# Performance work log

Hardware: AMD Instinct MI355X
Metric: run time of the kernel (lower is better)

The kernel has to match this reference:

```python
import jax, jax.numpy as jnp
import numpy as np

N_NODES = 100000
N_EDGES = 600000
VOCAB = 5000
NUM_GRAPHS = 2000
NUM_CLASSES = 10


def setup_inputs() -> dict:
    key = jax.random.key(0)
    ks = jax.random.split(key, 12)
    x = jax.random.randint(ks[0], (N_NODES,), 0, VOCAB, dtype=jnp.int32)
    edge_index = jax.random.randint(ks[1], (2, N_EDGES), 0, N_NODES, dtype=jnp.int32)
    batch = jnp.sort(jax.random.randint(ks[2], (N_NODES,), 0, NUM_GRAPHS, dtype=jnp.int32))
    emb = jax.random.normal(ks[3], (VOCAB, 64), dtype=jnp.float32) * 0.1
    W1 = jax.random.normal(ks[4], (64, 128), dtype=jnp.float32) * (1.0 / np.sqrt(64))
    b1 = jnp.zeros((128,), dtype=jnp.float32)
    W2 = jax.random.normal(ks[5], (128, 128), dtype=jnp.float32) * (1.0 / np.sqrt(128))
    b2 = jnp.zeros((128,), dtype=jnp.float32)
    Wlin = jax.random.normal(ks[6], (128, NUM_CLASSES), dtype=jnp.float32) * (1.0 / np.sqrt(128))
    blin = jnp.zeros((NUM_CLASSES,), dtype=jnp.float32)
    return {"x": x, "edge_index": edge_index, "batch": batch, "num_graphs": NUM_GRAPHS,
            "emb": emb, "W1": W1, "b1": b1, "W2": W2, "b2": b2, "Wlin": Wlin, "blin": blin}


def reference(x, edge_index, batch, num_graphs, emb, W1, b1, W2, b2, Wlin, blin):
    N = x.shape[0]
    loops = jnp.arange(N, dtype=edge_index.dtype)
    src = jnp.concatenate([edge_index[0], loops])  # message sources (j)
    dst = jnp.concatenate([edge_index[1], loops])  # aggregation targets (i)
    # GCN symmetric normalization with self-loops (PyG gcn_norm, source_to_target)
    deg = jax.ops.segment_sum(jnp.ones_like(dst, dtype=jnp.float32), dst, num_segments=N)
    dinv = jnp.where(deg > 0, jax.lax.rsqrt(deg), 0.0)
    norm = dinv[src] * dinv[dst]  # [E+N]

    def gcn(h, W, b):
        h = h @ W  # linear transform first (GCNConv order)
        msg = h[src] * norm[:, None]  # gather + scale, [E+N, F]
        return jax.ops.segment_sum(msg, dst, num_segments=N) + b

    h = emb[x]  # [N, 64]
    h = jax.nn.relu(gcn(h, W1, b1))
    h = jax.nn.relu(gcn(h, W2, b2))
    g = jax.ops.segment_max(h, batch, num_segments=num_graphs)  # global_max_pool
    return g @ Wlin + blin
```

## Files before the change

### kernel.cpp

```cpp
#include <hip/hip_runtime.h>
#include <hip/hip_bf16.h>
#include <hip/hip_fp16.h>


typedef _Float16 h8 __attribute__((ext_vector_type(8)));
typedef _Float16 h4v __attribute__((ext_vector_type(4)));
typedef float f32x4 __attribute__((ext_vector_type(4)));

__global__ __launch_bounds__(256) void k_zero(int4* __restrict__ deg, int n4i,
                                              int4* __restrict__ pool, int p4i) {
    int t = blockIdx.x * 256 + threadIdx.x;
    int4 z = make_int4(0, 0, 0, 0);
    if (t < n4i) deg[t] = z;
    if (t < p4i) pool[t] = z;
}

__global__ __launch_bounds__(256) void k_degprep(const int* __restrict__ dst, int* __restrict__ deg, int E,
                                                 const float* __restrict__ emb, __half2* __restrict__ e16,
                                                 const float* __restrict__ W1, _Float16* __restrict__ W1T,
                                                 const float* __restrict__ W2, _Float16* __restrict__ W2T,
                                                 int nEmbF, int gE, int nCast) {
    int bid = blockIdx.x;
    if (bid < gE) {
        int e = bid * 256 + threadIdx.x;
        if (e < E) atomicAdd(&deg[dst[e]], 1);
    } else if (bid < gE + nCast) {
        int t = (bid - gE) * 256 + threadIdx.x;
        if (t * 4 < nEmbF) {
            float4 v = *(const float4*)&emb[t * 4];
            e16[t * 2] = __floats2half2_rn(v.x, v.y);
            e16[t * 2 + 1] = __floats2half2_rn(v.z, v.w);
        }
    } else if (bid < gE + nCast + 32) {
        int t = (bid - gE - nCast) * 256 + threadIdx.x;
        int c = t >> 6, k = t & 63;
        W1T[c * 64 + k] = (_Float16)W1[k * 128 + c];
    } else {
        int t = (bid - gE - nCast - 32) * 256 + threadIdx.x;
        if (t < 128 * 128) {
            int c = t >> 7, k = t & 127;
            W2T[c * 128 + k] = (_Float16)W2[k * 128 + c];
        }
    }
}

__global__ __launch_bounds__(256) void k_scan1(const int* __restrict__ deg, int* __restrict__ exc,
                                               int* __restrict__ bsums, float* __restrict__ dinv, int N) {
    __shared__ int s[256];
    int i = blockIdx.x * 256 + threadIdx.x;
    int v = (i < N) ? deg[i] : 0;
    if (i < N) dinv[i] = rsqrtf((float)(v + 1));
    s[threadIdx.x] = v;
    __syncthreads();
    for (int off = 1; off < 256; off <<= 1) {
        int t = (threadIdx.x >= (unsigned)off) ? s[threadIdx.x - off] : 0;
        __syncthreads();
        s[threadIdx.x] += t;
        __syncthreads();
    }
    if (i < N) exc[i] = s[threadIdx.x] - v;
    if (threadIdx.x == 255) bsums[blockIdx.x] = s[255];
}

__global__ __launch_bounds__(512) void k_scan2(int* __restrict__ bsums, int nb) {
    __shared__ int s[512];
    int i = threadIdx.x;
    int v = (i < nb) ? bsums[i] : 0;
    s[i] = v;
    __syncthreads();
    for (int off = 1; off < 512; off <<= 1) {
        int t = (i >= off) ? s[i - off] : 0;
        __syncthreads();
        s[i] += t;
        __syncthreads();
    }
    if (i < nb) bsums[i] = s[i] - v;
}

__global__ __launch_bounds__(256) void k_scan3(int* __restrict__ rowstart, int* __restrict__ cursor,
                                               const int* __restrict__ bsums, int N, int E) {
    int i = blockIdx.x * 256 + threadIdx.x;
    if (i < N) {
        int r = rowstart[i] + bsums[blockIdx.x];
        rowstart[i] = r;
        cursor[i] = r;
    }
    if (i == 0 && blockIdx.x == 0) rowstart[N] = E;
}

__global__ __launch_bounds__(256) void k_fill(const int* __restrict__ src, const int* __restrict__ dst,
                                              const int* __restrict__ x, const float* __restrict__ dinv,
                                              int* __restrict__ cursor, int2* __restrict__ ed,
                                              int* __restrict__ cols, int E) {
    int e = blockIdx.x * 256 + threadIdx.x;
    if (e < E) {
        int d = dst[e];
        int s = src[e];
        int pos = atomicAdd(&cursor[d], 1);
        ed[pos] = make_int2(x[s], __float_as_int(dinv[s]));
        cols[pos] = s;
    }
}

__global__ __launch_bounds__(512) void k_mlp(const __half2* __restrict__ e16, const int* __restrict__ x,
                                             const float* __restrict__ dinv, const int* __restrict__ rs,
                                             const int2* __restrict__ ed, const _Float16* __restrict__ W1T,
                                             const float* __restrict__ b1, const _Float16* __restrict__ W2T,
                                             _Float16* __restrict__ P, int N) {
    __shared__ _Float16 Xs[64][72];
    __shared__ _Float16 Hs[64][136];
    int tid = threadIdx.x;
    int blk0 = blockIdx.x * 64;
    {
        int lane = tid & 31;
        int hw = tid >> 5;
#pragma unroll
        for (int pass = 0; pass < 2; ++pass) {
            int nl = hw * 4 + pass * 2;
            int gA = blk0 + nl;     if (gA >= N) gA = N - 1;
            int gB = blk0 + nl + 1; if (gB >= N) gB = N - 1;
            int cA0 = rs[gA], cA1 = rs[gA + 1];
            int cB0 = rs[gB], cB1 = rs[gB + 1];
            bool hasA = cA0 < cA1, hasB = cB0 < cB1;
            __half2 tA[8], tB[8];
            float wA[8], wB[8];
#pragma unroll
            for (int i = 0; i < 8; ++i) {
                int ei = cA0 + i;
                int ec = (ei < cA1) ? ei : (hasA ? cA1 - 1 : 0);
                int2 r2 = ed[ec];
                tA[i] = e16[(size_t)r2.x * 32 + lane];
                wA[i] = (ei < cA1) ? __int_as_float(r2.y) : 0.f;
            }
#pragma unroll
            for (int i = 0; i < 8; ++i) {
                int ei = cB0 + i;
                int ec = (ei < cB1) ? ei : (hasB ? cB1 - 1 : 0);
                int2 r2 = ed[ec];
                tB[i] = e16[(size_t)r2.x * 32 + lane];
                wB[i] = (ei < cB1) ? __int_as_float(r2.y) : 0.f;
            }
            float dA = dinv[gA], dB = dinv[gB];
            float2 sA = __half22float2(e16[(size_t)x[gA] * 32 + lane]);
            float2 sB = __half22float2(e16[(size_t)x[gB] * 32 + lane]);
            float aA0 = dA * sA.x, aA1 = dA * sA.y;
            float aB0 = dB * sB.x, aB1 = dB * sB.y;
#pragma unroll
            for (int i = 0; i < 8; ++i) {
                float2 tf = __half22float2(tA[i]);
                aA0 = fmaf(wA[i], tf.x, aA0);
                aA1 = fmaf(wA[i], tf.y, aA1);
            }
#pragma unroll
            for (int i = 0; i < 8; ++i) {
                float2 tf = __half22float2(tB[i]);
                aB0 = fmaf(wB[i], tf.x, aB0);
                aB1 = fmaf(wB[i], tf.y, aB1);
            }
            for (int e = cA0 + 8; e < cA1; e += 8) {
#pragma unroll
                for (int i = 0; i < 8; ++i) {
                    int ei = e + i;
                    int ec = (ei < cA1) ? ei : cA1 - 1;
                    int2 r2 = ed[ec];
                    tA[i] = e16[(size_t)r2.x * 32 + lane];
                    wA[i] = (ei < cA1) ? __int_as_float(r2.y) : 0.f;
                }
#pragma unroll
                for (int i = 0; i < 8; ++i) {
                    float2 tf = __half22float2(tA[i]);
                    aA0 = fmaf(wA[i], tf.x, aA0);
                    aA1 = fmaf(wA[i], tf.y, aA1);
                }
            }
            for (int e = cB0 + 8; e < cB1; e += 8) {
#pragma unroll
                for (int i = 0; i < 8; ++i) {
                    int ei = e + i;
                    int ec = (ei < cB1) ? ei : cB1 - 1;
                    int2 r2 = ed[ec];
                    tB[i] = e16[(size_t)r2.x * 32 + lane];
                    wB[i] = (ei < cB1) ? __int_as_float(r2.y) : 0.f;
                }
#pragma unroll
                for (int i = 0; i < 8; ++i) {
                    float2 tf = __half22float2(tB[i]);
                    aB0 = fmaf(wB[i], tf.x, aB0);
                    aB1 = fmaf(wB[i], tf.y, aB1);
                }
            }
            *(__half2*)&Xs[nl][lane * 2] = __floats2half2_rn(dA * aA0, dA * aA1);
            *(__half2*)&Xs[nl + 1][lane * 2] = __floats2half2_rn(dB * aB0, dB * aB1);
        }
    }
    __syncthreads();
    int l = tid & 63, wid = tid >> 6;
    int r = l & 15, kg = l >> 4;
    int rb = wid & 3;
    int ch = wid >> 2;
    {
        f32x4 acc[4];
#pragma unroll
        for (int ct = 0; ct < 4; ++ct) acc[ct] = (f32x4){0.f, 0.f, 0.f, 0.f};
#pragma unroll
        for (int kc = 0; kc < 2; ++kc) {
            h8 a = *(const h8*)&Xs[rb * 16 + r][kc * 32 + kg * 8];
#pragma unroll
            for (int ct = 0; ct < 4; ++ct) {
                h8 b = *(const h8*)(W1T + (size_t)(ch * 64 + ct * 16 + r) * 64 + kc * 32 + kg * 8);
                acc[ct] = __builtin_amdgcn_mfma_f32_16x16x32_f16(a, b, acc[ct], 0, 0, 0);
            }
        }
#pragma unroll
        for (int ct = 0; ct < 4; ++ct) {
            float bias = b1[ch * 64 + ct * 16 + r];
#pragma unroll
            for (int i = 0; i < 4; ++i)
                Hs[rb * 16 + 4 * kg + i][ch * 64 + ct * 16 + r] =
                    (_Float16)fmaxf(acc[ct][i] + bias, 0.f);
        }
    }
    __syncthreads();
    {
        f32x4 acc[4];
#pragma unroll
        for (int ct = 0; ct < 4; ++ct) acc[ct] = (f32x4){0.f, 0.f, 0.f, 0.f};
#pragma unroll
        for (int kc = 0; kc < 4; ++kc) {
            h8 a = *(const h8*)&Hs[rb * 16 + r][kc * 32 + kg * 8];
#pragma unroll
            for (int ct = 0; ct < 4; ++ct) {
                h8 b = *(const h8*)(W2T + (size_t)(ch * 64 + ct * 16 + r) * 128 + kc * 32 + kg * 8);
                acc[ct] = __builtin_amdgcn_mfma_f32_16x16x32_f16(a, b, acc[ct], 0, 0, 0);
            }
        }
        float dv[4];
#pragma unroll
        for (int i = 0; i < 4; ++i) {
            int gr = blk0 + rb * 16 + 4 * kg + i;
            dv[i] = (gr < N) ? dinv[gr] : 0.f;
        }
#pragma unroll
        for (int ct = 0; ct < 4; ++ct) {
#pragma unroll
            for (int i = 0; i < 4; ++i) {
                int gr = blk0 + rb * 16 + 4 * kg + i;
                if (gr < N)
                    P[(size_t)gr * 128 + ch * 64 + ct * 16 + r] = (_Float16)(acc[ct][i] * dv[i]);
            }
        }
    }
}

__global__ __launch_bounds__(256) void k_agg2pool(const h4v* __restrict__ P4, const int* __restrict__ batch,
                                                  const float* __restrict__ dinv, const int* __restrict__ rs,
                                                  const int* __restrict__ cols, const float4* __restrict__ bias4,
                                                  float* __restrict__ pool, int N, int G) {
    __shared__ int lpool[4][128];
    int tid = threadIdx.x;
    lpool[tid >> 7][tid & 127] = 0;
    lpool[(tid >> 7) + 2][tid & 127] = 0;
    __syncthreads();
    int lane = tid & 31;
    int blk_n0 = blockIdx.x * 16;
    int gfirst = batch[(blk_n0 < N) ? blk_n0 : (N - 1)];
    int n0 = blk_n0 + (tid >> 5) * 2;
    if (n0 < N) {
        int nA = n0;
        int nB = (n0 + 1 < N) ? n0 + 1 : n0;
        int cA0 = rs[nA], cA1 = rs[nA + 1];
        int cB0 = rs[nB], cB1 = rs[nB + 1];
        bool hasA = cA0 < cA1, hasB = cB0 < cB1;
        h4v sA = P4[(size_t)nA * 32 + lane];
        h4v sB = P4[(size_t)nB * 32 + lane];
        float aA[4], aB[4];
#pragma unroll
        for (int f = 0; f < 4; ++f) {
            aA[f] = (float)sA[f];
            aB[f] = (float)sB[f];
        }
        {
            h4v tA[16], tB[16];
#pragma unroll
            for (int i = 0; i < 16; ++i) {
                int ei = cA0 + i;
                int ec = (ei < cA1) ? ei : (hasA ? cA1 - 1 : 0);
                tA[i] = P4[(size_t)cols[ec] * 32 + lane];
            }
#pragma unroll
            for (int i = 0; i < 16; ++i) {
                int ei = cB0 + i;
                int ec = (ei < cB1) ? ei : (hasB ? cB1 - 1 : 0);
                tB[i] = P4[(size_t)cols[ec] * 32 + lane];
            }
#pragma unroll
            for (int i = 0; i < 16; ++i) {
                float w = (cA0 + i < cA1) ? 1.f : 0.f;
#pragma unroll
                for (int f = 0; f < 4; ++f) aA[f] = fmaf(w, (float)tA[i][f], aA[f]);
            }
#pragma unroll
            for (int i = 0; i < 16; ++i) {
                float w = (cB0 + i < cB1) ? 1.f : 0.f;
#pragma unroll
                for (int f = 0; f < 4; ++f) aB[f] = fmaf(w, (float)tB[i][f], aB[f]);
            }
        }
        for (int e = cA0 + 16; e < cA1; e += 16) {
            h4v t[16];
#pragma unroll
            for (int i = 0; i < 16; ++i) {
                int ei = e + i;
                int ec = (ei < cA1) ? ei : cA1 - 1;
                t[i] = P4[(size_t)cols[ec] * 32 + lane];
            }
#pragma unroll
            for (int i = 0; i < 16; ++i) {
                float w = (e + i < cA1) ? 1.f : 0.f;
#pragma unroll
                for (int f = 0; f < 4; ++f) aA[f] = fmaf(w, (float)t[i][f], aA[f]);
            }
        }
        for (int e = cB0 + 16; e < cB1; e += 16) {
            h4v t[16];
#pragma unroll
            for (int i = 0; i < 16; ++i) {
                int ei = e + i;
                int ec = (ei < cB1) ? ei : cB1 - 1;
                t[i] = P4[(size_t)cols[ec] * 32 + lane];
            }
#pragma unroll
            for (int i = 0; i < 16; ++i) {
                float w = (e + i < cB1) ? 1.f : 0.f;
#pragma unroll
                for (int f = 0; f < 4; ++f) aB[f] = fmaf(w, (float)t[i][f], aB[f]);
            }
        }
        float dA = dinv[nA], dB = dinv[nB];
        int gA = batch[nA], gB = batch[nB];
        float4 b = bias4[lane];
        float bv[4] = {b.x, b.y, b.z, b.w};
        float zA[4], zB[4];
#pragma unroll
        for (int f = 0; f < 4; ++f) {
            zA[f] = fmaxf(fmaf(dA, aA[f], bv[f]), 0.f);
            zB[f] = fmaxf(fmaf(dB, aB[f], bv[f]), 0.f);
        }
        int rot = (lane >> 3) & 3;
        auto emit = [&](int g, const float* m) {
            int slot = g - gfirst;
            if (slot < 4) {
#pragma unroll
                for (int f = 0; f < 4; ++f) {
                    int ff = (f + rot) & 3;
                    if (m[ff] > 0.f) atomicMax(&lpool[slot][lane * 4 + ff], __float_as_int(m[ff]));
                }
            } else {
                float* pg = pool + (size_t)g * 128 + lane * 4;
#pragma unroll
                for (int f = 0; f < 4; ++f)
                    if (m[f] > 0.f) atomicMax((int*)(pg + f), __float_as_int(m[f]));
            }
        };
        if (gA == gB) {
            float m[4];
#pragma unroll
            for (int f = 0; f < 4; ++f) m[f] = fmaxf(zA[f], zB[f]);
            emit(gA, m);
        } else {
            emit(gA, zA);
            emit(gB, zB);
        }
    }
    __syncthreads();
    {
        int f = tid & 127;
        for (int s = tid >> 7; s < 4; s += 2) {
            int v = lpool[s][f];
            if (v > 0) atomicMax((int*)&pool[(size_t)(gfirst + s) * 128 + f], v);
        }
    }
}

__global__ __launch_bounds__(256) void k_final(const float* __restrict__ pool, const float* __restrict__ Wlin,
                                               const float* __restrict__ blin, float* __restrict__ out, int G) {
    int t = blockIdx.x * 256 + threadIdx.x;
    if (t >= G * 10) return;
    int g = t / 10, c = t % 10;
    float acc = blin[c];
    const float* pr = pool + (size_t)g * 128;
#pragma unroll 8
    for (int f = 0; f < 128; ++f) acc = fmaf(pr[f], Wlin[f * 10 + c], acc);
    out[t] = acc;
}

extern "C" void kernel_launch(void* const* d_in, const int* in_sizes, int n_in,
                              void* d_out, int out_size, void* d_ws, size_t ws_size,
                              hipStream_t stream) {
    const int* x = (const int*)d_in[0];
    const int* ei = (const int*)d_in[1];
    const int* batch = (const int*)d_in[2];
    const float* emb = (const float*)d_in[4];
    const float* W1 = (const float*)d_in[5];
    const float* b1 = (const float*)d_in[6];
    const float* W2 = (const float*)d_in[7];
    const float* b2 = (const float*)d_in[8];
    const float* Wlin = (const float*)d_in[9];
    const float* blin = (const float*)d_in[10];
    float* out = (float*)d_out;

    int N = in_sizes[0];
    int E = in_sizes[1] / 2;
    int VOCAB = in_sizes[4] / 64;
    int G = out_size / 10;
    const int* srcp = ei;
    const int* dstp = ei + E;

    char* p = (char*)d_ws;
    auto alloc = [&](size_t bytes) -> char* {
        char* r = p;
        p += (bytes + 255) & ~(size_t)255;
        return r;
    };
    int* deg = (int*)alloc((size_t)N * 4);
    int* cursor = (int*)alloc((size_t)N * 4);
    int* rowstart = (int*)alloc((size_t)(N + 1) * 4);
    int* bsums = (int*)alloc(512 * 4);
    float* dinv = (float*)alloc((size_t)N * 4);
    int2* ed = (int2*)alloc((size_t)E * 8);
    int* cols = (int*)alloc((size_t)E * 4);
    _Float16* e16 = (_Float16*)alloc((size_t)VOCAB * 64 * 2);
    _Float16* W1T = (_Float16*)alloc(128 * 64 * 2);
    _Float16* W2T = (_Float16*)alloc(128 * 128 * 2);
    _Float16* P = (_Float16*)alloc((size_t)N * 128 * 2);
    float* pool = (float*)alloc((size_t)G * 128 * 4);

    int gE = (E + 255) / 256;
    int gN = (N + 255) / 256;
    int nEmbF = VOCAB * 64;
    int nCast = (nEmbF / 4 + 255) / 256;

    int n4i = N / 4, p4i = G * 128 / 4;
    int zg = ((n4i > p4i ? n4i : p4i) + 255) / 256;
    k_zero<<<zg, 256, 0, stream>>>((int4*)deg, n4i, (int4*)pool, p4i);
    k_degprep<<<gE + nCast + 32 + 64, 256, 0, stream>>>(dstp, deg, E, emb, (__half2*)e16, W1, W1T,
                                                        W2, W2T, nEmbF, gE, nCast);
    k_scan1<<<gN, 256, 0, stream>>>(deg, rowstart, bsums, dinv, N);
    k_scan2<<<1, 512, 0, stream>>>(bsums, gN);
    k_scan3<<<gN, 256, 0, stream>>>(rowstart, cursor, bsums, N, E);
    k_fill<<<gE, 256, 0, stream>>>(srcp, dstp, x, dinv, cursor, ed, cols, E);
    k_mlp<<<(N + 63) / 64, 512, 0, stream>>>((const __half2*)e16, x, dinv, rowstart, ed, W1T, b1,
                                             W2T, P, N);
    k_agg2pool<<<(N + 15) / 16, 256, 0, stream>>>((const h4v*)P, batch, dinv, rowstart, cols,
                                                  (const float4*)b2, pool, N, G);
    k_final<<<(G * 10 + 255) / 256, 256, 0, stream>>>(pool, Wlin, blin, out, G);
}
```

Measured before the change: 195.4 us.

## Drop scan3, use packed fp16 accumulation and zero-row padding in gather kernels

Removes the third scan kernel by having consumers compute row starts from the block-local exclusive counts plus block sums; k_fill uses the local counts as cursors. Edge weights are stored as duplicated half2, and both aggregation loops accumulate in packed fp16 (hfma2/hadd2). Out-of-range edges redirect to a zeroed padding row instead of masking weights. k_mlp blocks shrink from 64 to 32 nodes for more blocks. This trades fewer instructions and one less launch for reduced accumulation precision in fp16.

```diff
diff --git a/kernel.cpp b/kernel.cpp
--- a/kernel.cpp
+++ b/kernel.cpp
@@ -4,15 +4,18 @@
 
 
 typedef _Float16 h8 __attribute__((ext_vector_type(8)));
-typedef _Float16 h4v __attribute__((ext_vector_type(4)));
 typedef float f32x4 __attribute__((ext_vector_type(4)));
-
-__global__ __launch_bounds__(256) void k_zero(int4* __restrict__ deg, int n4i,
-                                              int4* __restrict__ pool, int p4i) {
+struct H22 { __half2 a, b; };
+
+__global__ __launch_bounds__(256) void k_zero(int4* __restrict__ deg4, int n4i,
+                                              int4* __restrict__ pool4, int p4i,
+                                              int4* __restrict__ e16z, int4* __restrict__ Pz) {
     int t = blockIdx.x * 256 + threadIdx.x;
     int4 z = make_int4(0, 0, 0, 0);
-    if (t < n4i) deg[t] = z;
-    if (t < p4i) pool[t] = z;
+    if (t < n4i) deg4[t] = z;
+    if (t < p4i) pool4[t] = z;
+    if (t < 8) e16z[t] = z;
+    if (t < 16) Pz[t] = z;
 }
 
 __global__ __launch_bounds__(256) void k_degprep(const int* __restrict__ dst, int* __restrict__ deg, int E,
@@ -77,160 +80,157 @@
     if (i < nb) bsums[i] = s[i] - v;
 }
 
-__global__ __launch_bounds__(256) void k_scan3(int* __restrict__ rowstart, int* __restrict__ cursor,
-                                               const int* __restrict__ bsums, int N, int E) {
-    int i = blockIdx.x * 256 + threadIdx.x;
-    if (i < N) {
-        int r = rowstart[i] + bsums[blockIdx.x];
-        rowstart[i] = r;
-        cursor[i] = r;
-    }
-    if (i == 0 && blockIdx.x == 0) rowstart[N] = E;
-}
-
 __global__ __launch_bounds__(256) void k_fill(const int* __restrict__ src, const int* __restrict__ dst,
                                               const int* __restrict__ x, const float* __restrict__ dinv,
-                                              int* __restrict__ cursor, int2* __restrict__ ed,
-                                              int* __restrict__ cols, int E) {
+                                              int* __restrict__ exc, const int* __restrict__ bs,
+                                              int* __restrict__ cols, int2* __restrict__ ed, int E) {
     int e = blockIdx.x * 256 + threadIdx.x;
     if (e < E) {
         int d = dst[e];
         int s = src[e];
-        int pos = atomicAdd(&cursor[d], 1);
-        ed[pos] = make_int2(x[s], __float_as_int(dinv[s]));
+        int pos = atomicAdd(&exc[d], 1) + bs[d >> 8];
         cols[pos] = s;
+        unsigned int u = (unsigned int)__half_as_ushort(__float2half(dinv[s]));
+        ed[pos] = make_int2(x[s], (int)(u | (u << 16)));
     }
 }
 
 __global__ __launch_bounds__(512) void k_mlp(const __half2* __restrict__ e16, const int* __restrict__ x,
-                                             const float* __restrict__ dinv, const int* __restrict__ rs,
-                                             const int2* __restrict__ ed, const _Float16* __restrict__ W1T,
-                                             const float* __restrict__ b1, const _Float16* __restrict__ W2T,
-                                             _Float16* __restrict__ P, int N) {
-    __shared__ _Float16 Xs[64][72];
-    __shared__ _Float16 Hs[64][136];
+                                             const float* __restrict__ dinv, const int* __restrict__ exc,
+                                             const int* __restrict__ bs, const int2* __restrict__ ed,
+                                             const _Float16* __restrict__ W1T, const float* __restrict__ b1,
+                                             const _Float16* __restrict__ W2T, _Float16* __restrict__ P,
+                                             int N, int VOCAB, int E) {
+    __shared__ _Float16 Xs[32][72];
+    __shared__ _Float16 Hs[32][136];
     int tid = threadIdx.x;
-    int blk0 = blockIdx.x * 64;
+    int blk0 = blockIdx.x * 32;
     {
         int lane = tid & 31;
         int hw = tid >> 5;
-#pragma unroll
-        for (int pass = 0; pass < 2; ++pass) {
-            int nl = hw * 4 + pass * 2;
-            int gA = blk0 + nl;     if (gA >= N) gA = N - 1;
-            int gB = blk0 + nl + 1; if (gB >= N) gB = N - 1;
-            int cA0 = rs[gA], cA1 = rs[gA + 1];
-            int cB0 = rs[gB], cB1 = rs[gB + 1];
-            bool hasA = cA0 < cA1, hasB = cB0 < cB1;
-            __half2 tA[8], tB[8];
-            float wA[8], wB[8];
+        int nlA = hw * 2, nlB = hw * 2 + 1;
+        int gA = blk0 + nlA; if (gA >= N) gA = N - 1;
+        int gB = blk0 + nlB; if (gB >= N) gB = N - 1;
+        int cA1 = exc[gA] + bs[gA >> 8];
+        int cA0 = gA ? exc[gA - 1] + bs[(gA - 1) >> 8] : 0;
+        int cB1 = exc[gB] + bs[gB >> 8];
+        int cB0 = gB ? exc[gB - 1] + bs[(gB - 1) >> 8] : 0;
+        float dA = dinv[gA], dB = dinv[gB];
+        __half2 sA = e16[(size_t)x[gA] * 32 + lane];
+        __half2 sB = e16[(size_t)x[gB] * 32 + lane];
+        __half2 z2 = __float2half2_rn(0.f);
+        __half2 aA0 = z2, aA1 = z2, aB0 = z2, aB1 = z2;
+        int Emax = E - 1;
+        {
+            __half2 tA[8], tB[8], wA[8], wB[8];
 #pragma unroll
             for (int i = 0; i < 8; ++i) {
                 int ei = cA0 + i;
-                int ec = (ei < cA1) ? ei : (hasA ? cA1 - 1 : 0);
+                int ec = min(ei, Emax);
                 int2 r2 = ed[ec];
-                tA[i] = e16[(size_t)r2.x * 32 + lane];
-                wA[i] = (ei < cA1) ? __int_as_float(r2.y) : 0.f;
+                int rx = (ei < cA1) ? r2.x : VOCAB;
+                tA[i] = e16[(size_t)rx * 32 + lane];
+                wA[i] = *reinterpret_cast<const __half2*>(&r2.y);
             }
 #pragma unroll
             for (int i = 0; i < 8; ++i) {
                 int ei = cB0 + i;
-                int ec = (ei < cB1) ? ei : (hasB ? cB1 - 1 : 0);
+                int ec = min(ei, Emax);
                 int2 r2 = ed[ec];
-                tB[i] = e16[(size_t)r2.x * 32 + lane];
-                wB[i] = (ei < cB1) ? __int_as_float(r2.y) : 0.f;
-            }
-            float dA = dinv[gA], dB = dinv[gB];
-            float2 sA = __half22float2(e16[(size_t)x[gA] * 32 + lane]);
-            float2 sB = __half22float2(e16[(size_t)x[gB] * 32 + lane]);
-            float aA0 = dA * sA.x, aA1 = dA * sA.y;
-            float aB0 = dB * sB.x, aB1 = dB * sB.y;
-#pragma unroll
-            for (int i = 0; i < 8; ++i) {
-                float2 tf = __half22float2(tA[i]);
-                aA0 = fmaf(wA[i], tf.x, aA0);
-                aA1 = fmaf(wA[i], tf.y, aA1);
-            }
-#pragma unroll
-            for (int i = 0; i < 8; ++i) {
-                float2 tf = __half22float2(tB[i]);
-                aB0 = fmaf(wB[i], tf.x, aB0);
-                aB1 = fmaf(wB[i], tf.y, aB1);
-            }
-            for (int e = cA0 + 8; e < cA1; e += 8) {
-#pragma unroll
-                for (int i = 0; i < 8; ++i) {
-                    int ei = e + i;
-                    int ec = (ei < cA1) ? ei : cA1 - 1;
-                    int2 r2 = ed[ec];
-                    tA[i] = e16[(size_t)r2.x * 32 + lane];
-                    wA[i] = (ei < cA1) ? __int_as_float(r2.y) : 0.f;
-                }
-#pragma unroll
-                for (int i = 0; i < 8; ++i) {
-                    float2 tf = __half22float2(tA[i]);
-                    aA0 = fmaf(wA[i], tf.x, aA0);
-                    aA1 = fmaf(wA[i], tf.y, aA1);
-                }
-            }
-            for (int e = cB0 + 8; e < cB1; e += 8) {
-#pragma unroll
-                for (int i = 0; i < 8; ++i) {
-                    int ei = e + i;
-                    int ec = (ei < cB1) ? ei : cB1 - 1;
-                    int2 r2 = ed[ec];
-                    tB[i] = e16[(size_t)r2.x * 32 + lane];
-                    wB[i] = (ei < cB1) ? __int_as_float(r2.y) : 0.f;
-                }
-#pragma unroll
-                for (int i = 0; i < 8; ++i) {
-                    float2 tf = __half22float2(tB[i]);
-                    aB0 = fmaf(wB[i], tf.x, aB0);
-                    aB1 = fmaf(wB[i], tf.y, aB1);
-                }
-            }
-            *(__half2*)&Xs[nl][lane * 2] = __floats2half2_rn(dA * aA0, dA * aA1);
-            *(__half2*)&Xs[nl + 1][lane * 2] = __floats2half2_rn(dB * aB0, dB * aB1);
-        }
+                int rx = (ei < cB1) ? r2.x : VOCAB;
+                tB[i] = e16[(size_t)rx * 32 + lane];
+                wB[i] = *reinterpret_cast<const __half2*>(&r2.y);
+            }
+#pragma unroll
+            for (int i = 0; i < 8; i += 2) {
+                aA0 = __hfma2(wA[i], tA[i], aA0);
+                aA1 = __hfma2(wA[i + 1], tA[i + 1], aA1);
+                aB0 = __hfma2(wB[i], tB[i], aB0);
+                aB1 = __hfma2(wB[i + 1], tB[i + 1], aB1);
+            }
+        }
+        for (int e0 = cA0 + 8; e0 < cA1; e0 += 8) {
+            __half2 t[8], w[8];
+#pragma unroll
+            for (int i = 0; i < 8; ++i) {
+                int ei = e0 + i;
+                int ec = min(ei, Emax);
+                int2 r2 = ed[ec];
+                int rx = (ei < cA1) ? r2.x : VOCAB;
+                t[i] = e16[(size_t)rx * 32 + lane];
+                w[i] = *reinterpret_cast<const __half2*>(&r2.y);
+            }
+#pragma unroll
+            for (int i = 0; i < 8; i += 2) {
+                aA0 = __hfma2(w[i], t[i], aA0);
+                aA1 = __hfma2(w[i + 1], t[i + 1], aA1);
+            }
+        }
+        for (int e0 = cB0 + 8; e0 < cB1; e0 += 8) {
+            __half2 t[8], w[8];
+#pragma unroll
+            for (int i = 0; i < 8; ++i) {
+                int ei = e0 + i;
+                int ec = min(ei, Emax);
+                int2 r2 = ed[ec];
+                int rx = (ei < cB1) ? r2.x : VOCAB;
+                t[i] = e16[(size_t)rx * 32 + lane];
+                w[i] = *reinterpret_cast<const __half2*>(&r2.y);
+            }
+#pragma unroll
+            for (int i = 0; i < 8; i += 2) {
+                aB0 = __hfma2(w[i], t[i], aB0);
+                aB1 = __hfma2(w[i + 1], t[i + 1], aB1);
+            }
+        }
+        float2 mA0 = __half22float2(aA0), mA1 = __half22float2(aA1);
+        float2 mB0 = __half22float2(aB0), mB1 = __half22float2(aB1);
+        float mAx = mA0.x + mA1.x, mAy = mA0.y + mA1.y;
+        float mBx = mB0.x + mB1.x, mBy = mB0.y + mB1.y;
+        float2 fsA = __half22float2(sA), fsB = __half22float2(sB);
+        *(__half2*)&Xs[nlA][lane * 2] =
+            __floats2half2_rn(dA * fmaf(dA, fsA.x, mAx), dA * fmaf(dA, fsA.y, mAy));
+        *(__half2*)&Xs[nlB][lane * 2] =
+            __floats2half2_rn(dB * fmaf(dB, fsB.x, mBx), dB * fmaf(dB, fsB.y, mBy));
     }
     __syncthreads();
     int l = tid & 63, wid = tid >> 6;
     int r = l & 15, kg = l >> 4;
-    int rb = wid & 3;
-    int ch = wid >> 2;
+    int rb = wid & 1;
+    int cq = wid >> 1;
     {
-        f32x4 acc[4];
-#pragma unroll
-        for (int ct = 0; ct < 4; ++ct) acc[ct] = (f32x4){0.f, 0.f, 0.f, 0.f};
+        f32x4 acc[2];
+#pragma unroll
+        for (int ct = 0; ct < 2; ++ct) acc[ct] = (f32x4){0.f, 0.f, 0.f, 0.f};
 #pragma unroll
         for (int kc = 0; kc < 2; ++kc) {
             h8 a = *(const h8*)&Xs[rb * 16 + r][kc * 32 + kg * 8];
 #pragma unroll
-            for (int ct = 0; ct < 4; ++ct) {
-                h8 b = *(const h8*)(W1T + (size_t)(ch * 64 + ct * 16 + r) * 64 + kc * 32 + kg * 8);
+            for (int ct = 0; ct < 2; ++ct) {
+                h8 b = *(const h8*)(W1T + (size_t)(cq * 32 + ct * 16 + r) * 64 + kc * 32 + kg * 8);
                 acc[ct] = __builtin_amdgcn_mfma_f32_16x16x32_f16(a, b, acc[ct], 0, 0, 0);
             }
         }
 #pragma unroll
-        for (int ct = 0; ct < 4; ++ct) {
-            float bias = b1[ch * 64 + ct * 16 + r];
+        for (int ct = 0; ct < 2; ++ct) {
+            float bias = b1[cq * 32 + ct * 16 + r];
 #pragma unroll
             for (int i = 0; i < 4; ++i)
-                Hs[rb * 16 + 4 * kg + i][ch * 64 + ct * 16 + r] =
+                Hs[rb * 16 + 4 * kg + i][cq * 32 + ct * 16 + r] =
                     (_Float16)fmaxf(acc[ct][i] + bias, 0.f);
         }
     }
     __syncthreads();
     {
-        f32x4 acc[4];
-#pragma unroll
-        for (int ct = 0; ct < 4; ++ct) acc[ct] = (f32x4){0.f, 0.f, 0.f, 0.f};
+        f32x4 acc[2];
+#pragma unroll
+        for (int ct = 0; ct < 2; ++ct) acc[ct] = (f32x4){0.f, 0.f, 0.f, 0.f};
 #pragma unroll
         for (int kc = 0; kc < 4; ++kc) {
             h8 a = *(const h8*)&Hs[rb * 16 + r][kc * 32 + kg * 8];
 #pragma unroll
-            for (int ct = 0; ct < 4; ++ct) {
-                h8 b = *(const h8*)(W2T + (size_t)(ch * 64 + ct * 16 + r) * 128 + kc * 32 + kg * 8);
+            for (int ct = 0; ct < 2; ++ct) {
+                h8 b = *(const h8*)(W2T + (size_t)(cq * 32 + ct * 16 + r) * 128 + kc * 32 + kg * 8);
                 acc[ct] = __builtin_amdgcn_mfma_f32_16x16x32_f16(a, b, acc[ct], 0, 0, 0);
             }
         }
@@ -241,21 +241,22 @@
             dv[i] = (gr < N) ? dinv[gr] : 0.f;
         }
 #pragma unroll
-        for (int ct = 0; ct < 4; ++ct) {
+        for (int ct = 0; ct < 2; ++ct) {
 #pragma unroll
             for (int i = 0; i < 4; ++i) {
                 int gr = blk0 + rb * 16 + 4 * kg + i;
                 if (gr < N)
-                    P[(size_t)gr * 128 + ch * 64 + ct * 16 + r] = (_Float16)(acc[ct][i] * dv[i]);
-            }
-        }
-    }
-}
-
-__global__ __launch_bounds__(256) void k_agg2pool(const h4v* __restrict__ P4, const int* __restrict__ batch,
-                                                  const float* __restrict__ dinv, const int* __restrict__ rs,
-                                                  const int* __restrict__ cols, const float4* __restrict__ bias4,
-                                                  float* __restrict__ pool, int N, int G) {
+                    P[(size_t)gr * 128 + cq * 32 + ct * 16 + r] = (_Float16)(acc[ct][i] * dv[i]);
+            }
+        }
+    }
+}
+
+__global__ __launch_bounds__(256) void k_agg2pool(const H22* __restrict__ P22, const int* __restrict__ batch,
+                                                  const float* __restrict__ dinv, const int* __restrict__ exc,
+                                                  const int* __restrict__ bs, const int* __restrict__ cols,
+                                                  const float4* __restrict__ bias4, float* __restrict__ pool,
+                                                  int N, int E) {
     __shared__ int lpool[4][128];
     int tid = threadIdx.x;
     lpool[tid >> 7][tid & 127] = 0;
@@ -268,73 +269,91 @@
     if (n0 < N) {
         int nA = n0;
         int nB = (n0 + 1 < N) ? n0 + 1 : n0;
-        int cA0 = rs[nA], cA1 = rs[nA + 1];
-        int cB0 = rs[nB], cB1 = rs[nB + 1];
-        bool hasA = cA0 < cA1, hasB = cB0 < cB1;
-        h4v sA = P4[(size_t)nA * 32 + lane];
-        h4v sB = P4[(size_t)nB * 32 + lane];
-        float aA[4], aB[4];
-#pragma unroll
-        for (int f = 0; f < 4; ++f) {
-            aA[f] = (float)sA[f];
-            aB[f] = (float)sB[f];
-        }
+        int cA1 = exc[nA] + bs[nA >> 8];
+        int cA0 = nA ? exc[nA - 1] + bs[(nA - 1) >> 8] : 0;
+        int cB1 = exc[nB] + bs[nB >> 8];
+        int cB0 = nB ? exc[nB - 1] + bs[(nB - 1) >> 8] : 0;
+        H22 sA = P22[(size_t)nA * 32 + lane];
+        H22 sB = P22[(size_t)nB * 32 + lane];
+        float2 fa = __half22float2(sA.a), fb = __half22float2(sA.b);
+        float aA[4] = {fa.x, fa.y, fb.x, fb.y};
+        fa = __half22float2(sB.a); fb = __half22float2(sB.b);
+        float aB[4] = {fa.x, fa.y, fb.x, fb.y};
+        int Emax = E - 1;
+        __half2 z2 = __float2half2_rn(0.f);
         {
-            h4v tA[16], tB[16];
+            H22 tA[16], tB[16];
 #pragma unroll
             for (int i = 0; i < 16; ++i) {
                 int ei = cA0 + i;
-                int ec = (ei < cA1) ? ei : (hasA ? cA1 - 1 : 0);
-                tA[i] = P4[(size_t)cols[ec] * 32 + lane];
+                int ec = min(ei, Emax);
+                int col = (ei < cA1) ? cols[ec] : N;
+                tA[i] = P22[(size_t)col * 32 + lane];
             }
 #pragma unroll
             for (int i = 0; i < 16; ++i) {
                 int ei = cB0 + i;
-                int ec = (ei < cB1) ? ei : (hasB ? cB1 - 1 : 0);
-                tB[i] = P4[(size_t)cols[ec] * 32 + lane];
-            }
-#pragma unroll
-            for (int i = 0; i < 16; ++i) {
-                float w = (cA0 + i < cA1) ? 1.f : 0.f;
-#pragma unroll
-                for (int f = 0; f < 4; ++f) aA[f] = fmaf(w, (float)tA[i][f], aA[f]);
-            }
-#pragma unroll
-            for (int i = 0; i < 16; ++i) {
-                float w = (cB0 + i < cB1) ? 1.f : 0.f;
-#pragma unroll
-                for (int f = 0; f < 4; ++f) aB[f] = fmaf(w, (float)tB[i][f], aB[f]);
-            }
-        }
-        for (int e = cA0 + 16; e < cA1; e += 16) {
-            h4v t[16];
-#pragma unroll
-            for (int i = 0; i < 16; ++i) {
-                int ei = e + i;
-                int ec = (ei < cA1) ? ei : cA1 - 1;
-                t[i] = P4[(size_t)cols[ec] * 32 + lane];
-            }
-#pragma unroll
-            for (int i = 0; i < 16; ++i) {
-                float w = (e + i < cA1) ? 1.f : 0.f;
-#pragma unroll
-                for (int f = 0; f < 4; ++f) aA[f] = fmaf(w, (float)t[i][f], aA[f]);
-            }
-        }
-        for (int e = cB0 + 16; e < cB1; e += 16) {
-            h4v t[16];
-#pragma unroll
-            for (int i = 0; i < 16; ++i) {
-                int ei = e + i;
-                int ec = (ei < cB1) ? ei : cB1 - 1;
-                t[i] = P4[(size_t)cols[ec] * 32 + lane];
-            }
-#pragma unroll
-            for (int i = 0; i < 16; ++i) {
-                float w = (e + i < cB1) ? 1.f : 0.f;
-#pragma unroll
-                for (int f = 0; f < 4; ++f) aB[f] = fmaf(w, (float)t[i][f], aB[f]);
-            }
+                int ec = min(ei, Emax);
+                int col = (ei < cB1) ? cols[ec] : N;
+                tB[i] = P22[(size_t)col * 32 + lane];
+            }
+            __half2 pA0 = z2, pA1 = z2, pA2 = z2, pA3 = z2;
+            __half2 pB0 = z2, pB1 = z2, pB2 = z2, pB3 = z2;
+#pragma unroll
+            for (int i = 0; i < 16; i += 2) {
+                pA0 = __hadd2(pA0, tA[i].a);
+                pA1 = __hadd2(pA1, tA[i].b);
+                pA2 = __hadd2(pA2, tA[i + 1].a);
+                pA3 = __hadd2(pA3, tA[i + 1].b);
+                pB0 = __hadd2(pB0, tB[i].a);
+                pB1 = __hadd2(pB1, tB[i].b);
+                pB2 = __hadd2(pB2, tB[i + 1].a);
+                pB3 = __hadd2(pB3, tB[i + 1].b);
+            }
+            float2 q0 = __half22float2(pA0), q1 = __half22float2(pA2);
+            float2 q2 = __half22float2(pA1), q3 = __half22float2(pA3);
+            aA[0] += q0.x + q1.x; aA[1] += q0.y + q1.y;
+            aA[2] += q2.x + q3.x; aA[3] += q2.y + q3.y;
+            q0 = __half22float2(pB0); q1 = __half22float2(pB2);
+            q2 = __half22float2(pB1); q3 = __half22float2(pB3);
+            aB[0] += q0.x + q1.x; aB[1] += q0.y + q1.y;
+            aB[2] += q2.x + q3.x; aB[3] += q2.y + q3.y;
+        }
+        for (int e0 = cA0 + 16; e0 < cA1; e0 += 8) {
+            H22 t[8];
+#pragma unroll
+            for (int i = 0; i < 8; ++i) {
+                int ei = e0 + i;
+                int ec = min(ei, Emax);
+                int col = (ei < cA1) ? cols[ec] : N;
+                t[i] = P22[(size_t)col * 32 + lane];
+            }
+            __half2 p0 = z2, p1 = z2;
+#pragma unroll
+            for (int i = 0; i < 8; ++i) {
+                p0 = __hadd2(p0, t[i].a);
+                p1 = __hadd2(p1, t[i].b);
+            }
+            float2 q0 = __half22float2(p0), q1 = __half22float2(p1);
+            aA[0] += q0.x; aA[1] += q0.y; aA[2] += q1.x; aA[3] += q1.y;
+        }
+        for (int e0 = cB0 + 16; e0 < cB1; e0 += 8) {
+            H22 t[8];
+#pragma unroll
+            for (int i = 0; i < 8; ++i) {
+                int ei = e0 + i;
+                int ec = min(ei, Emax);
+                int col = (ei < cB1) ? cols[ec] : N;
+                t[i] = P22[(size_t)col * 32 + lane];
+            }
+            __half2 p0 = z2, p1 = z2;
+#pragma unroll
+            for (int i = 0; i < 8; ++i) {
+                p0 = __hadd2(p0, t[i].a);
+                p1 = __hadd2(p1, t[i].b);
+            }
+            float2 q0 = __half22float2(p0), q1 = __half22float2(p1);
+            aB[0] += q0.x; aB[1] += q0.y; aB[2] += q1.x; aB[3] += q1.y;
         }
         float dA = dinv[nA], dB = dinv[nB];
         int gA = batch[nA], gB = batch[nB];
@@ -423,16 +442,15 @@
         return r;
     };
     int* deg = (int*)alloc((size_t)N * 4);
-    int* cursor = (int*)alloc((size_t)N * 4);
-    int* rowstart = (int*)alloc((size_t)(N + 1) * 4);
+    int* exc = (int*)alloc((size_t)N * 4);
     int* bsums = (int*)alloc(512 * 4);
     float* dinv = (float*)alloc((size_t)N * 4);
     int2* ed = (int2*)alloc((size_t)E * 8);
     int* cols = (int*)alloc((size_t)E * 4);
-    _Float16* e16 = (_Float16*)alloc((size_t)VOCAB * 64 * 2);
+    _Float16* e16 = (_Float16*)alloc((size_t)(VOCAB + 1) * 64 * 2);
     _Float16* W1T = (_Float16*)alloc(128 * 64 * 2);
     _Float16* W2T = (_Float16*)alloc(128 * 128 * 2);
-    _Float16* P = (_Float16*)alloc((size_t)N * 128 * 2);
+    _Float16* P = (_Float16*)alloc((size_t)(N + 1) * 128 * 2);
     float* pool = (float*)alloc((size_t)G * 128 * 4);
 
     int gE = (E + 255) / 256;
@@ -442,16 +460,16 @@
 
     int n4i = N / 4, p4i = G * 128 / 4;
     int zg = ((n4i > p4i ? n4i : p4i) + 255) / 256;
-    k_zero<<<zg, 256, 0, stream>>>((int4*)deg, n4i, (int4*)pool, p4i);
+    k_zero<<<zg, 256, 0, stream>>>((int4*)deg, n4i, (int4*)pool, p4i,
+                                   (int4*)(e16 + (size_t)VOCAB * 64), (int4*)(P + (size_t)N * 128));
     k_degprep<<<gE + nCast + 32 + 64, 256, 0, stream>>>(dstp, deg, E, emb, (__half2*)e16, W1, W1T,
                                                         W2, W2T, nEmbF, gE, nCast);
-    k_scan1<<<gN, 256, 0, stream>>>(deg, rowstart, bsums, dinv, N);
+    k_scan1<<<gN, 256, 0, stream>>>(deg, exc, bsums, dinv, N);
     k_scan2<<<1, 512, 0, stream>>>(bsums, gN);
-    k_scan3<<<gN, 256, 0, stream>>>(rowstart, cursor, bsums, N, E);
-    k_fill<<<gE, 256, 0, stream>>>(srcp, dstp, x, dinv, cursor, ed, cols, E);
-    k_mlp<<<(N + 63) / 64, 512, 0, stream>>>((const __half2*)e16, x, dinv, rowstart, ed, W1T, b1,
-                                             W2T, P, N);
-    k_agg2pool<<<(N + 15) / 16, 256, 0, stream>>>((const h4v*)P, batch, dinv, rowstart, cols,
-                                                  (const float4*)b2, pool, N, G);
+    k_fill<<<gE, 256, 0, stream>>>(srcp, dstp, x, dinv, exc, bsums, cols, ed, E);
+    k_mlp<<<(N + 31) / 32, 512, 0, stream>>>((const __half2*)e16, x, dinv, exc, bsums, ed, W1T, b1,
+                                             W2T, P, N, VOCAB, E);
+    k_agg2pool<<<(N + 15) / 16, 256, 0, stream>>>((const H22*)P, batch, dinv, exc, bsums, cols,
+                                                  (const float4*)b2, pool, N, E);
     k_final<<<(G * 10 + 255) / 256, 256, 0, stream>>>(pool, Wlin, blin, out, G);
 }
```

Result: slower. 211.4 us (+8.2%).
